# Optimization experiments

Hardware: AMD Instinct MI355X
Metric: run time of the kernel (lower is better)

The kernel has to match this reference:

```python
import jax, jax.numpy as jnp
import numpy as np

B, L, D, H, V = 4, 128, 128, 8, 32000
N_ITER = 4
DAMP_H = DAMP_Z = DAMP_X = 0.0
STEP_H = STEP_Z = STEP_X = 1.0
REG_H = REG_Z = REG_X = 1.0
BLOCK_MSG = False
NEG = 1e9


def _norm(t):
    # norm='softmax'
    return jax.nn.softmax(t, axis=-1)


def setup_inputs() -> dict:
    key = jax.random.key(0)
    k1, k2, k3, k4 = jax.random.split(key, 4)
    x = jax.random.normal(k1, (B, L, D), dtype=jnp.float32)
    mask = jnp.ones((B, L), dtype=jnp.int32)
    m_mask = jax.random.randint(k2, (B, L), 0, 2).astype(jnp.int32)
    embed_matrix = jax.random.normal(k3, (V, D), dtype=jnp.float32)
    ternary = jax.random.normal(k4, (2, D, D, H), dtype=jnp.float32)  # dists='' -> 2 groups
    return {"x": x, "mask": mask, "embed_matrix": embed_matrix, "m_mask": m_mask, "ternary": ternary}


def _forward(x, mask, embed_matrix, m_mask, ternary):
    dt = x.dtype
    mask1d = mask != 0                                   # [B,L] True = real token
    valid2d = mask1d[:, :, None] & mask1d[:, None, :]    # [B,L,L]
    inv2d = ~valid2d[:, None, :, :]                      # broadcast over heads
    keep = mask1d[..., None].astype(dt)                  # [B,L,1]
    mm = m_mask.astype(dt)[..., None]                    # [B,L,1]

    # distance mask: dists='' -> [triu(1); tril(-1)] -> [2,L,L]
    dm = jnp.triu(jnp.ones((L, L), dt), 1)
    distmask = jnp.stack([dm, dm.T], axis=0)

    eye = jnp.eye(L, dtype=dt)

    unary = x
    q_x = jnp.ones((B, L, V), dt)
    # initialize_Z=True: masked positions start from expected embedding
    pre = _norm(q_x) @ embed_matrix                      # [B,L,D]
    q_z = unary * (1.0 - mm) + pre * mm
    q_z = q_z * keep

    q_h = jnp.ones((B, H, L, L), dt) - eye * NEG
    q_h = jnp.where(inv2d, -NEG, q_h)

    cache_qh, cache_qz, cache_qx = q_h, q_z, q_x
    # async_update=True: normalize Z before first H update
    q_z = _norm(q_z) * keep

    for _ in range(N_ITER):
        # ---- H update: F[z,c,i,j] = sum_{k,a,b} q_z[z,i,a] q_z[z,j,b] T[k,a,b,c] dist[k,i,j]
        t1 = jnp.einsum('zia,kabc->zkibc', q_z, ternary)            # [B,2,L,D,H]
        F = jnp.einsum('zkibc,zjb,kij->zcij', t1, q_z, distmask)    # [B,H,L,L]
        q_h = cache_qh * DAMP_H + F * (1.0 - DAMP_H) / REG_H
        q_h = cache_qh * (1.0 - STEP_H) + q_h * STEP_H
        cache_qh = q_h
        q_h = q_h - eye * NEG
        q_h = jnp.where(inv2d, -NEG, q_h)
        q_hn = _norm(q_h)                                           # [B,H,L,L]

        # ---- Z update: first-order messages from ternary factors
        m = q_hn[:, None] * distmask[None, :, None]                 # [B,2,H,L,L]
        s1 = jnp.einsum('zkcij,zjb->zkibc', m, q_z)                 # to Z_i (head slot)
        G = jnp.einsum('zkibc,kabc->zia', s1, ternary)
        if not BLOCK_MSG:
            s2 = jnp.einsum('zkcij,zia->zkjac', m, q_z)             # to Z_j (dep slot)
            G = G + jnp.einsum('zkjac,kabc->zjb', s2, ternary)

        # unary: X message replaces word unary at <MASK> positions
        unary_eff = unary * (1.0 - mm) + (_norm(q_x) @ embed_matrix) * mm
        q_z_new = cache_qz * DAMP_Z + (unary_eff + G) * (1.0 - DAMP_Z) / REG_Z
        q_z_new = cache_qz * (1.0 - STEP_Z) + q_z_new * STEP_Z
        cache_qz = q_z_new
        q_z = _norm(q_z_new) * keep

        # ---- X update: message from Z through embedding factor
        msg_x = jnp.einsum('zia,va->ziv', q_z, embed_matrix)        # [B,L,V]
        q_x_new = cache_qx * DAMP_X + msg_x * (1.0 - DAMP_X) / REG_X
        q_x_new = cache_qx * (1.0 - STEP_X) + q_x_new * STEP_X
        cache_qx = q_x_new
        q_x = q_x_new

    # output_prob=False -> unnormalized scores
    return q_x


def reference(x, mask, embed_matrix, m_mask, ternary):
    return _forward(x, mask, embed_matrix, m_mask, ternary)
```

## Files before the change

### kernel.cpp

```cpp
#include <hip/hip_runtime.h>
#include <math.h>

#define L_ 128
#define D_ 128
#define H_ 8
#define V_ 32000
#define NEGC 1e9f

typedef short short8 __attribute__((ext_vector_type(8)));
typedef float f32x4 __attribute__((ext_vector_type(4)));
typedef unsigned short ushort8v __attribute__((ext_vector_type(8)));

__device__ __forceinline__ unsigned short f2bf(float x) {
    unsigned int u = __float_as_uint(x);
    unsigned int r = (u + 0x7fff + ((u >> 16) & 1)) >> 16;
    return (unsigned short)r;
}


__global__ __launch_bounds__(256) void prep_k(const float* __restrict__ E,
                                              unsigned short* __restrict__ Ebf,
                                              unsigned short* __restrict__ Etf,
                                              const float* __restrict__ T, float* __restrict__ Tt,
                                              const int* __restrict__ m_mask,
                                              int* __restrict__ rowidx, int* __restrict__ nactb,
                                              float* __restrict__ meansum) {
    __shared__ __align__(16) unsigned char psmem[8704];
    int blk = blockIdx.x;
    int t = threadIdx.x;
    if (blk < 1000) {
        unsigned short* tile = (unsigned short*)psmem;
        int v0 = blk * 32;
#pragma unroll
        for (int i = 0; i < 4; ++i) {
            int idx = i * 256 + t;
            int v = idx >> 5;
            int d4 = (idx & 31) * 4;
            float4 val = *(const float4*)&E[(size_t)(v0 + v) * 128 + d4];
            tile[v * 136 + d4 + 0] = f2bf(val.x);
            tile[v * 136 + d4 + 1] = f2bf(val.y);
            tile[v * 136 + d4 + 2] = f2bf(val.z);
            tile[v * 136 + d4 + 3] = f2bf(val.w);
        }
        __syncthreads();
        {
            int fi = t >> 5;
            int l0 = (t & 31) * 2;
            int vtl = fi >> 2, s = fi & 3;
            size_t base = ((size_t)(blk * 2 + vtl) * 4 + s) * 512;
#pragma unroll
            for (int li = 0; li < 2; ++li) {
                int l = l0 + li;
                int nl = l & 15, hf = l >> 4;
                ushort8v o;
#pragma unroll
                for (int j = 0; j < 8; ++j) o[j] = tile[(vtl * 16 + nl) * 136 + s * 32 + hf * 8 + j];
                *(ushort8v*)&Ebf[base + l * 8] = o;
            }
        }
        {
            int ct = t >> 5;
            int l0 = (t & 31) * 2;
            size_t base = ((size_t)blk * 8 + ct) * 512;
#pragma unroll
            for (int li = 0; li < 2; ++li) {
                int l = l0 + li;
                int nl = l & 15, hf = l >> 4;
                ushort8v o;
#pragma unroll
                for (int j = 0; j < 8; ++j) o[j] = tile[(hf * 8 + j) * 136 + ct * 16 + nl];
                *(ushort8v*)&Etf[base + l * 8] = o;
            }
        }
    } else if (blk < 1256) {
        int tb = blk - 1000;
        for (int q = 0; q < 4; ++q) {
            int id = tb * 1024 + q * 256 + t;
            int k = id >> 17;
            int rem = id & 131071;
            int a = rem >> 10;
            int bc = rem & 1023;
            int b = bc >> 3, c = bc & 7;
            Tt[k * 131072 + b * 1024 + a * 8 + c] = T[id];
        }
    } else if (blk == 1256) {
        int* wc = (int*)psmem;
        bool a0 = m_mask[t] != 0;
        bool a1 = m_mask[t + 256] != 0;
        unsigned long long b0 = __ballot(a0);
        unsigned long long b1 = __ballot(a1);
        int w = t >> 6, lane = t & 63;
        if (lane == 0) { wc[w] = __popcll(b0); wc[4 + w] = __popcll(b1); }
        __syncthreads();
        int base0 = 0;
        for (int i = 0; i < w; ++i) base0 += wc[i];
        int base1 = 0;
        for (int i = 0; i < 4 + w; ++i) base1 += wc[i];
        if (a0) rowidx[base0 + __popcll(b0 & ((1ull << lane) - 1))] = t;
        if (a1) rowidx[base1 + __popcll(b1 & ((1ull << lane) - 1))] = t + 256;
        if (t == 0) {
            int tot = 0;
            for (int i = 0; i < 8; ++i) tot += wc[i];
            nactb[0] = tot;
        }
    } else {
        float* red = (float*)psmem;
        int d = t & 127, h = t >> 7;
        int v0 = (blk - 1257) * 256;
        float s = 0.f;
        for (int p = 0; p < 128; ++p)
            s += E[(size_t)(v0 + h + 2 * p) * 128 + d];
        red[t] = s;
        __syncthreads();
        if (h == 0) atomicAdd(&meansum[d], red[d] + red[128 + d]);
    }
}

__global__ __launch_bounds__(64) void init_k(const float* __restrict__ x, const int* __restrict__ mask,
                                             const int* __restrict__ m_mask, const float* __restrict__ meansum,
                                             float* __restrict__ ue, float* __restrict__ qz,
                                             unsigned short* __restrict__ qzb) {
    int row = blockIdx.x, t = threadIdx.x;
    float keepv = mask[row] ? 1.f : 0.f;
    bool mm = m_mask[row] != 0;
    float pre0 = meansum[t] * (1.f / 32000.f);
    float pre1 = meansum[t + 64] * (1.f / 32000.f);
    float u0 = mm ? pre0 : x[row * 128 + t];
    float u1 = mm ? pre1 : x[row * 128 + t + 64];
    ue[row * 128 + t] = u0;
    ue[row * 128 + t + 64] = u1;
    float sv0 = u0 * keepv, sv1 = u1 * keepv;
    float m = fmaxf(sv0, sv1);
    for (int off = 32; off; off >>= 1) m = fmaxf(m, __shfl_xor(m, off));
    float e0 = __expf(sv0 - m), e1 = __expf(sv1 - m);
    float s = e0 + e1;
    for (int off = 32; off; off >>= 1) s += __shfl_xor(s, off);
    float inv = keepv / s;
    float q0 = e0 * inv, q1 = e1 * inv;
    qz[row * 128 + t] = q0;
    qz[row * 128 + t + 64] = q1;
    qzb[row * 128 + t] = f2bf(q0);
    qzb[row * 128 + t + 64] = f2bf(q1);
}


__global__ __launch_bounds__(256) void fusedA_k(const float* __restrict__ qz, const float* __restrict__ T,
                                                const float* __restrict__ Tt, float* __restrict__ U2,
                                                unsigned short* __restrict__ Ut, unsigned short* __restrict__ Wt,
                                                const unsigned short* __restrict__ qzb,
                                                const unsigned short* __restrict__ Ebf,
                                                const unsigned short* __restrict__ Etf,
                                                const int* __restrict__ rowidx, const int* __restrict__ nactb,
                                                float* __restrict__ partial, float* __restrict__ partial_rs) {
    __shared__ __align__(16) unsigned char smem[42752];
    int blk = blockIdx.x;
    int t = threadIdx.x;
    if (blk < 512) {
        float* aL = (float*)smem;
        int by = blk >> 5;
        int uw = by >> 3, z = (by >> 1) & 3, k = by & 1;
        int bx = blk & 31;
        int m0 = (bx >> 2) * 16, n = (bx & 3) * 256 + t;
        const float* A = qz + z * 16384;
        const float* Bm = (uw ? Tt : T) + k * 131072;
        for (int idx = t; idx < 2048; idx += 256)
            aL[idx] = A[(m0 + (idx >> 7)) * 128 + (idx & 127)];
        __syncthreads();
        float acc[16];
#pragma unroll
        for (int m = 0; m < 16; ++m) acc[m] = 0.f;
        for (int kq = 0; kq < 32; ++kq) {
            float b0 = Bm[(kq * 4 + 0) * 1024 + n];
            float b1 = Bm[(kq * 4 + 1) * 1024 + n];
            float b2 = Bm[(kq * 4 + 2) * 1024 + n];
            float b3 = Bm[(kq * 4 + 3) * 1024 + n];
#pragma unroll
            for (int m = 0; m < 16; ++m) {
                const float4 aq = *(const float4*)&aL[m * 128 + kq * 4];
                acc[m] += aq.x * b0 + aq.y * b1 + aq.z * b2 + aq.w * b3;
            }
        }
        if (uw == 0) {
            float* Cm = U2 + (z * 2 + k) * 131072;
#pragma unroll
            for (int m = 0; m < 16; ++m)
                Cm[(m0 + m) * 1024 + n] = acc[m];
        }
        int bb = n >> 3, cc = n & 7;
        ushort8v p0, p1;
#pragma unroll
        for (int m = 0; m < 8; ++m) { p0[m] = f2bf(acc[m]); p1[m] = f2bf(acc[8 + m]); }
        unsigned short* To = (uw ? Wt : Ut) + ((size_t)(z * 2 + k) * 128 + bb) * 1024 + cc * 128 + m0;
        *(ushort8v*)&To[0] = p0;
        *(ushort8v*)&To[8] = p1;
    } else {
        int nact = nactb[0];
        int bid = blk - 512;
        int xcd = bid & 7, idx = bid >> 3;
        int g = xcd + 8 * (idx >> 5);
        int bx = idx & 31;
        int r0 = bx * 16;
        if (g >= 50 || r0 >= nact) return;
        unsigned short* Pl = (unsigned short*)smem;
        float* slab = (float*)(smem + 9216);
        float* rsW  = (float*)(smem + 9216 + 33280);
        int w = t >> 6, lane = t & 63;
        int nloc = lane & 15, half = lane >> 4;
        int rA = r0 + nloc;
        bool actA = rA < nact;
        int rowA = actA ? rowidx[rA] : 0;
        short8 zero8 = (short8){0, 0, 0, 0, 0, 0, 0, 0};
        short8 afr[4];
#pragma unroll
        for (int s = 0; s < 4; ++s) {
            short8 v = *(const short8*)&qzb[rowA * 128 + s * 32 + half * 8];
            afr[s] = actA ? v : zero8;
        }
        const int kc0 = g * 20 + w * 5;
        short8 ebb[2][8];
#pragma unroll
        for (int f = 0; f < 8; ++f)
            ebb[0][f] = *(const short8*)&Ebf[((size_t)(kc0 * 8 + f)) * 512 + lane * 8];
        f32x4 acc2[8];
#pragma unroll
        for (int ct = 0; ct < 8; ++ct) acc2[ct] = (f32x4){0.f, 0.f, 0.f, 0.f};
        float rsl = 0.f;
#pragma unroll
        for (int step = 0; step < 5; ++step) {
            const int p = step & 1;
            const int kc = kc0 + step;
            short8 et[8];
#pragma unroll
            for (int f = 0; f < 8; ++f)
                et[f] = *(const short8*)&Etf[((size_t)(kc * 8 + f)) * 512 + lane * 8];
            if (step < 4) {
#pragma unroll
                for (int f = 0; f < 8; ++f)
                    ebb[p ^ 1][f] = *(const short8*)&Ebf[((size_t)((kc + 1) * 8 + f)) * 512 + lane * 8];
            }
            f32x4 p0 = (f32x4){0.f, 0.f, 0.f, 0.f};
            f32x4 p1 = (f32x4){0.f, 0.f, 0.f, 0.f};
#pragma unroll
            for (int s = 0; s < 4; ++s) {
                p0 = __builtin_amdgcn_mfma_f32_16x16x32_bf16(ebb[p][s], afr[s], p0, 0, 0, 0);
                p1 = __builtin_amdgcn_mfma_f32_16x16x32_bf16(ebb[p][4 + s], afr[s], p1, 0, 0, 0);
            }
            unsigned short* pw = Pl + (w * 2 + p) * 576;
            {
                float e0 = __expf(p0[0]), e1 = __expf(p0[1]), e2 = __expf(p0[2]), e3 = __expf(p0[3]);
                rsl += (e0 + e1) + (e2 + e3);
                uint2 pk = {(unsigned)f2bf(e0) | ((unsigned)f2bf(e1) << 16),
                            (unsigned)f2bf(e2) | ((unsigned)f2bf(e3) << 16)};
                *(uint2*)&pw[nloc * 36 + half * 4] = pk;
            }
            {
                float e0 = __expf(p1[0]), e1 = __expf(p1[1]), e2 = __expf(p1[2]), e3 = __expf(p1[3]);
                rsl += (e0 + e1) + (e2 + e3);
                uint2 pk = {(unsigned)f2bf(e0) | ((unsigned)f2bf(e1) << 16),
                            (unsigned)f2bf(e2) | ((unsigned)f2bf(e3) << 16)};
                *(uint2*)&pw[nloc * 36 + 16 + half * 4] = pk;
            }
            short8 a2 = *(const short8*)&pw[nloc * 36 + half * 8];
#pragma unroll
            for (int ct = 0; ct < 8; ++ct)
                acc2[ct] = __builtin_amdgcn_mfma_f32_16x16x32_bf16(a2, et[ct], acc2[ct], 0, 0, 0);
        }
        rsl += __shfl_xor(rsl, 16);
        rsl += __shfl_xor(rsl, 32);
        if (lane < 16) rsW[w * 16 + nloc] = rsl;
#pragma unroll
        for (int ct = 0; ct < 8; ++ct)
#pragma unroll
            for (int reg = 0; reg < 4; ++reg)
                slab[w * 2080 + (half * 4 + reg) * 130 + ct * 16 + nloc] = acc2[ct][reg];
        __syncthreads();
        float* pb = partial + (size_t)g * 65536;
        for (int i = t; i < 2048; i += 256) {
            int row = i >> 7, col = i & 127;
            int rr = r0 + row;
            if (rr < nact)
                pb[rr * 128 + col] = slab[row * 130 + col] + slab[2080 + row * 130 + col]
                                   + slab[4160 + row * 130 + col] + slab[6240 + row * 130 + col];
        }
        if (t < 16) {
            int rr = r0 + t;
            if (rr < nact)
                partial_rs[g * 512 + rr] = rsW[t] + rsW[16 + t] + rsW[32 + t] + rsW[48 + t];
        }
    }
}

__global__ __launch_bounds__(256) void fusedB_k(const float* __restrict__ qz, const float* __restrict__ U2,
                                                const int* __restrict__ mask,
                                                unsigned short* __restrict__ A0b, unsigned short* __restrict__ A1b,
                                                unsigned short* __restrict__ A0Tb, unsigned short* __restrict__ A1Tb,
                                                const float* __restrict__ partial, const float* __restrict__ partial_rs,
                                                const int* __restrict__ rowidx, const int* __restrict__ nactb,
                                                float* __restrict__ exbuf, float* __restrict__ rowsum) {
    __shared__ __align__(16) unsigned char smem[23552];
    int blk = blockIdx.x;
    int t = threadIdx.x;
    if (blk >= 256) {
        int nact = nactb[0];
        int idx = (blk - 256) * 256 + t;
        int rr = idx >> 7, col = idx & 127;
        if (rr >= nact) return;
        float s = 0.f;
#pragma unroll 10
        for (int g = 0; g < 50; ++g)
            s += partial[(size_t)g * 65536 + rr * 128 + col];
        int row = rowidx[rr];
        exbuf[row * 128 + col] = s;
        if (col == 0) {
            float ts = 0.f;
#pragma unroll 10
            for (int g = 0; g < 50; ++g) ts += partial_rs[g * 512 + rr];
            rowsum[row] = ts;
        }
        return;
    }
    float* As = (float*)smem;
    float* Bs = (float*)(smem + 4608);
    int* maskL = (int*)(smem + 4608 + 18432);
    int z = blk >> 6, c = (blk >> 3) & 7, iq = blk & 7;
    int i0 = iq * 16;
    int tj = t & 15, ti = t >> 4;
    int i = i0 + ti;
    if (t < 128) maskL[t] = mask[z * 128 + t];
    float acc0[8], acc1[8];
#pragma unroll
    for (int jj = 0; jj < 8; ++jj) { acc0[jj] = 0.f; acc1[jj] = 0.f; }
    const float* U2z = U2 + (size_t)z * 262144;
    const float* qzz = qz + z * 16384;
    for (int kb = 0; kb < 4; ++kb) {
        int b0 = kb * 32;
        __syncthreads();
        for (int e = t; e < 1024; e += 256) {
            int k = e >> 9, r = e & 511, ii = r >> 5, b = r & 31;
            As[(k * 16 + ii) * 36 + b] = U2z[k * 131072 + (i0 + ii) * 1024 + (b0 + b) * 8 + c];
        }
        for (int f = t; f < 1024; f += 256) {
            int j = f >> 3, b4 = f & 7;
            int slot = b4 ^ ((j >> 3) & 7);
            *(float4*)&Bs[j * 36 + slot * 4] = *(const float4*)&qzz[j * 128 + b0 + b4 * 4];
        }
        __syncthreads();
#pragma unroll
        for (int b4 = 0; b4 < 8; ++b4) {
            float4 a0 = *(const float4*)&As[(0 * 16 + ti) * 36 + b4 * 4];
            float4 a1 = *(const float4*)&As[(1 * 16 + ti) * 36 + b4 * 4];
#pragma unroll
            for (int jj = 0; jj < 8; ++jj) {
                int j = tj * 8 + jj;
                int slot = b4 ^ ((j >> 3) & 7);
                float4 bq = *(const float4*)&Bs[j * 36 + slot * 4];
                acc0[jj] += a0.x * bq.x;
                acc0[jj] += a0.y * bq.y;
                acc0[jj] += a0.z * bq.z;
                acc0[jj] += a0.w * bq.w;
                acc1[jj] += a1.x * bq.x;
                acc1[jj] += a1.y * bq.y;
                acc1[jj] += a1.z * bq.z;
                acc1[jj] += a1.w * bq.w;
            }
        }
    }
    bool vi = maskL[i] != 0;
    float fv[8];
#pragma unroll
    for (int jj = 0; jj < 8; ++jj) {
        int j2 = tj * 8 + jj;
        float F = (j2 > i) ? acc0[jj] : acc1[jj];
        if (j2 == i) F -= NEGC;
        if (!vi || maskL[j2] == 0) F = -NEGC;
        fv[jj] = F;
    }
    float mval = fv[0];
#pragma unroll
    for (int jj = 1; jj < 8; ++jj) mval = fmaxf(mval, fv[jj]);
    for (int off = 1; off < 16; off <<= 1) mval = fmaxf(mval, __shfl_xor(mval, off));
    float ssum = 0.f;
#pragma unroll
    for (int jj = 0; jj < 8; ++jj) ssum += __expf(fv[jj] - mval);
    for (int off = 1; off < 16; off <<= 1) ssum += __shfl_xor(ssum, off);
    float inv = 1.f / ssum;
    size_t base = (size_t)(z * 8 + c) * 16384;
    ushort8v v0, v1;
    unsigned short bvv[8];
#pragma unroll
    for (int jj = 0; jj < 8; ++jj) {
        int j2 = tj * 8 + jj;
        float val = __expf(fv[jj] - mval) * inv;
        unsigned short bv = f2bf(val);
        bvv[jj] = bv;
        v0[jj] = (j2 > i) ? bv : (unsigned short)0;
        v1[jj] = (j2 < i) ? bv : (unsigned short)0;
    }
    *(ushort8v*)&A0b[base + i * 128 + tj * 8] = v0;
    *(ushort8v*)&A1b[base + i * 128 + tj * 8] = v1;
#pragma unroll
    for (int jj = 0; jj < 8; ++jj) {
        int j2 = tj * 8 + jj;
        A0Tb[base + j2 * 128 + i] = (i < j2) ? bvv[jj] : (unsigned short)0;
        A1Tb[base + j2 * 128 + i] = (i > j2) ? bvv[jj] : (unsigned short)0;
    }
}

__global__ __launch_bounds__(64) void gkern_mfma_k(const unsigned short* __restrict__ A0b,
                                                   const unsigned short* __restrict__ A1b,
                                                   const unsigned short* __restrict__ A0Tb,
                                                   const unsigned short* __restrict__ A1Tb,
                                                   const unsigned short* __restrict__ Ut,
                                                   const unsigned short* __restrict__ Wt,
                                                   float* __restrict__ g1, float* __restrict__ g2) {
    int mode = blockIdx.y;
    int bx = blockIdx.x;
    int z = bx >> 6, it = (bx >> 3) & 7, at = bx & 7;
    int lane = threadIdx.x;
    int nloc = lane & 15, half = lane >> 4;
    int i0 = it * 16, a0 = at * 16;
    const unsigned short* Am0 = (mode ? A0Tb : A0b) + (size_t)z * 131072;
    const unsigned short* Am1 = (mode ? A1Tb : A1b) + (size_t)z * 131072;
    const unsigned short* Bt = mode ? Ut : Wt;
    const unsigned short* B0 = Bt + (size_t)(z * 2 + 0) * 131072 + (size_t)(a0 + nloc) * 1024;
    const unsigned short* B1 = Bt + (size_t)(z * 2 + 1) * 131072 + (size_t)(a0 + nloc) * 1024;
    const unsigned short* Ar0 = Am0 + (size_t)(i0 + nloc) * 128;
    const unsigned short* Ar1 = Am1 + (size_t)(i0 + nloc) * 128;
    f32x4 acc = (f32x4){0.f, 0.f, 0.f, 0.f};
#pragma unroll
    for (int c = 0; c < 8; ++c) {
#pragma unroll
        for (int sb = 0; sb < 4; ++sb) {
            int s0 = sb * 32 + half * 8;
            short8 av0 = *(const short8*)&Ar0[c * 16384 + s0];
            short8 bv0 = *(const short8*)&B0[c * 128 + s0];
            acc = __builtin_amdgcn_mfma_f32_16x16x32_bf16(av0, bv0, acc, 0, 0, 0);
            short8 av1 = *(const short8*)&Ar1[c * 16384 + s0];
            short8 bv1 = *(const short8*)&B1[c * 128 + s0];
            acc = __builtin_amdgcn_mfma_f32_16x16x32_bf16(av1, bv1, acc, 0, 0, 0);
        }
    }
    float* G = mode ? g2 : g1;
#pragma unroll
    for (int reg = 0; reg < 4; ++reg)
        G[(z * 128 + i0 + half * 4 + reg) * 128 + a0 + nloc] = acc[reg];
}

__global__ __launch_bounds__(64) void zupd_k(const float* __restrict__ ue, const float* __restrict__ x,
                                             const int* __restrict__ m_mask,
                                             const float* __restrict__ exbuf, const float* __restrict__ rowsum,
                                             const float* __restrict__ g1, const float* __restrict__ g2,
                                             const int* __restrict__ mask,
                                             float* __restrict__ qz, unsigned short* __restrict__ qzb, int useEx) {
    int row = blockIdx.x, t = threadIdx.x;
    float keepv = mask[row] ? 1.f : 0.f;
    int b = row * 128;
    float u0, u1;
    if (useEx) {
        if (m_mask[row] != 0) {
            float rsv = rowsum[row];
            u0 = exbuf[b + t] / rsv;
            u1 = exbuf[b + t + 64] / rsv;
        } else {
            u0 = x[b + t];
            u1 = x[b + t + 64];
        }
    } else {
        u0 = ue[b + t];
        u1 = ue[b + t + 64];
    }
    float v0 = u0 + g1[b + t] + g2[b + t];
    float v1 = u1 + g1[b + t + 64] + g2[b + t + 64];
    float m = fmaxf(v0, v1);
    for (int off = 32; off; off >>= 1) m = fmaxf(m, __shfl_xor(m, off));
    float e0 = __expf(v0 - m), e1 = __expf(v1 - m);
    float s = e0 + e1;
    for (int off = 32; off; off >>= 1) s += __shfl_xor(s, off);
    float inv = keepv / s;
    float q0 = e0 * inv, q1 = e1 * inv;
    qz[b + t] = q0;
    qz[b + t + 64] = q1;
    qzb[b + t] = f2bf(q0);
    qzb[b + t + 64] = f2bf(q1);
}

__global__ __launch_bounds__(256) void msgx_mfma_k(const unsigned short* __restrict__ qzb,
                                                   const unsigned short* __restrict__ Ebf,
                                                   float* __restrict__ out) {
    int t = threadIdx.x;
    int w = t >> 6, lane = t & 63;
    int nloc = lane & 15, half = lane >> 4;
    int rt0 = blockIdx.x * 64;
    int cb0 = blockIdx.y * 256 + w * 64;
    short8 afr[4][4];
#pragma unroll
    for (int r = 0; r < 4; ++r)
#pragma unroll
        for (int s = 0; s < 4; ++s)
            afr[r][s] = *(const short8*)&qzb[(rt0 + r * 16 + nloc) * 128 + s * 32 + half * 8];
    f32x4 acc[4][4];
#pragma unroll
    for (int r = 0; r < 4; ++r)
#pragma unroll
        for (int ct = 0; ct < 4; ++ct)
            acc[r][ct] = (f32x4){0.f, 0.f, 0.f, 0.f};
#pragma unroll
    for (int ct = 0; ct < 4; ++ct) {
#pragma unroll
        for (int s = 0; s < 4; ++s) {
            short8 bfr = *(const short8*)&Ebf[(((size_t)(cb0 >> 4) + ct) * 4 + s) * 512 + lane * 8];
#pragma unroll
            for (int r = 0; r < 4; ++r)
                acc[r][ct] = __builtin_amdgcn_mfma_f32_16x16x32_bf16(afr[r][s], bfr, acc[r][ct], 0, 0, 0);
        }
    }
#pragma unroll
    for (int r = 0; r < 4; ++r)
#pragma unroll
        for (int ct = 0; ct < 4; ++ct) {
            int col = cb0 + ct * 16 + nloc;
#pragma unroll
            for (int reg = 0; reg < 4; ++reg) {
                int row = rt0 + r * 16 + half * 4 + reg;
                out[(size_t)row * V_ + col] = acc[r][ct][reg];
            }
        }
}

extern "C" void kernel_launch(void* const* d_in, const int* in_sizes, int n_in,
                              void* d_out, int out_size, void* d_ws, size_t ws_size,
                              hipStream_t stream) {
    const float* x     = (const float*)d_in[0];
    const int*   mask  = (const int*)d_in[1];
    const float* E     = (const float*)d_in[2];
    const int*   mmask = (const int*)d_in[3];
    const float* T     = (const float*)d_in[4];
    float* out = (float*)d_out;

    float* w = (float*)d_ws;
    float* meansum = w;
    float* ue      = w + 128;
    float* qz      = ue + 65536;
    float* exbuf   = qz + 65536;
    float* rowsum  = exbuf + 65536;
    float* g1      = rowsum + 512;
    float* g2      = g1 + 65536;
    float* Tt      = g2 + 65536;
    float* U2      = Tt + 262144;
    float* prs     = U2 + 1048576;
    unsigned short* qzb  = (unsigned short*)(prs + 25600);
    unsigned short* Ebf  = qzb + 65536;
    unsigned short* Etf  = Ebf + 4096000;
    unsigned short* A0b  = Etf + 4096000;
    unsigned short* A1b  = A0b + 524288;
    unsigned short* A0Tb = A1b + 524288;
    unsigned short* A1Tb = A0Tb + 524288;
    unsigned short* Ut   = A1Tb + 524288;
    unsigned short* Wt   = Ut + 1048576;
    int* rowidx = (int*)(Wt + 1048576);
    int* nactb  = rowidx + 512;

    float* partial = out;

    hipMemsetAsync(meansum, 0, 128 * sizeof(float), stream);
    prep_k<<<1382, 256, 0, stream>>>(E, Ebf, Etf, T, Tt, mmask, rowidx, nactb, meansum);
    init_k<<<512, 64, 0, stream>>>(x, mask, mmask, meansum, ue, qz, qzb);

    for (int it = 0; it < 4; ++it) {
        fusedA_k<<<it ? 2304 : 512, 256, 0, stream>>>(qz, T, Tt, U2, Ut, Wt,
                                                      qzb, Ebf, Etf, rowidx, nactb, partial, prs);
        fusedB_k<<<it ? 512 : 256, 256, 0, stream>>>(qz, U2, mask, A0b, A1b, A0Tb, A1Tb,
                                                     partial, prs, rowidx, nactb, exbuf, rowsum);
        gkern_mfma_k<<<dim3(256, 2), 64, 0, stream>>>(A0b, A1b, A0Tb, A1Tb, Ut, Wt, g1, g2);
        zupd_k<<<512, 64, 0, stream>>>(ue, x, mmask, exbuf, rowsum, g1, g2, mask, qz, qzb, it ? 1 : 0);
    }
    msgx_mfma_k<<<dim3(8, 125), 256, 0, stream>>>(qzb, Ebf, out);
}
```

Before: 377.3 us.

## Double per-thread columns in fusedA GEMM and replace meansum atomics with partial sums

The fusedA GEMM branch now has each thread compute two output columns (n0 and n0+256), which halves the block count from 512 to 256 and reuses each shared-memory A load across twice the work. Separately, the embedding column-mean reduction writes per-block partial sums to a buffer instead of doing atomicAdd. init_k then sums the 125 partials itself, which also removes the memset launch. The cost is more registers per thread and fewer blocks for latency hiding, and every init block now repeats the 125-way partial sum.

```diff
diff --git a/kernel.cpp b/kernel.cpp
--- a/kernel.cpp
+++ b/kernel.cpp
@@ -24,7 +24,7 @@
                                               const float* __restrict__ T, float* __restrict__ Tt,
                                               const int* __restrict__ m_mask,
                                               int* __restrict__ rowidx, int* __restrict__ nactb,
-                                              float* __restrict__ meansum) {
+                                              float* __restrict__ cs) {
     __shared__ __align__(16) unsigned char psmem[8704];
     int blk = blockIdx.x;
     int t = threadIdx.x;
@@ -105,26 +105,33 @@
         }
     } else {
         float* red = (float*)psmem;
+        int pblk = blk - 1257;
         int d = t & 127, h = t >> 7;
-        int v0 = (blk - 1257) * 256;
+        int v0 = pblk * 256;
         float s = 0.f;
         for (int p = 0; p < 128; ++p)
             s += E[(size_t)(v0 + h + 2 * p) * 128 + d];
         red[t] = s;
         __syncthreads();
-        if (h == 0) atomicAdd(&meansum[d], red[d] + red[128 + d]);
+        if (h == 0) cs[pblk * 128 + d] = red[d] + red[128 + d];
     }
 }
 
 __global__ __launch_bounds__(64) void init_k(const float* __restrict__ x, const int* __restrict__ mask,
-                                             const int* __restrict__ m_mask, const float* __restrict__ meansum,
+                                             const int* __restrict__ m_mask, const float* __restrict__ cs,
                                              float* __restrict__ ue, float* __restrict__ qz,
                                              unsigned short* __restrict__ qzb) {
     int row = blockIdx.x, t = threadIdx.x;
     float keepv = mask[row] ? 1.f : 0.f;
     bool mm = m_mask[row] != 0;
-    float pre0 = meansum[t] * (1.f / 32000.f);
-    float pre1 = meansum[t + 64] * (1.f / 32000.f);
+    float s0 = 0.f, s1 = 0.f;
+#pragma unroll 5
+    for (int p = 0; p < 125; ++p) {
+        s0 += cs[p * 128 + t];
+        s1 += cs[p * 128 + t + 64];
+    }
+    float pre0 = s0 * (1.f / 32000.f);
+    float pre1 = s1 * (1.f / 32000.f);
     float u0 = mm ? pre0 : x[row * 128 + t];
     float u1 = mm ? pre1 : x[row * 128 + t + 64];
     ue[row * 128 + t] = u0;
@@ -155,47 +162,68 @@
     __shared__ __align__(16) unsigned char smem[42752];
     int blk = blockIdx.x;
     int t = threadIdx.x;
-    if (blk < 512) {
+    if (blk < 256) {
         float* aL = (float*)smem;
-        int by = blk >> 5;
+        int by = blk >> 4;
         int uw = by >> 3, z = (by >> 1) & 3, k = by & 1;
-        int bx = blk & 31;
-        int m0 = (bx >> 2) * 16, n = (bx & 3) * 256 + t;
+        int bx = blk & 15;
+        int m0 = (bx >> 1) * 16;
+        int n0 = (bx & 1) * 512 + t;
         const float* A = qz + z * 16384;
         const float* Bm = (uw ? Tt : T) + k * 131072;
         for (int idx = t; idx < 2048; idx += 256)
             aL[idx] = A[(m0 + (idx >> 7)) * 128 + (idx & 127)];
         __syncthreads();
-        float acc[16];
-#pragma unroll
-        for (int m = 0; m < 16; ++m) acc[m] = 0.f;
+        float acc0[16], acc1[16];
+#pragma unroll
+        for (int m = 0; m < 16; ++m) { acc0[m] = 0.f; acc1[m] = 0.f; }
         for (int kq = 0; kq < 32; ++kq) {
-            float b0 = Bm[(kq * 4 + 0) * 1024 + n];
-            float b1 = Bm[(kq * 4 + 1) * 1024 + n];
-            float b2 = Bm[(kq * 4 + 2) * 1024 + n];
-            float b3 = Bm[(kq * 4 + 3) * 1024 + n];
+            float b00 = Bm[(kq * 4 + 0) * 1024 + n0];
+            float b10 = Bm[(kq * 4 + 1) * 1024 + n0];
+            float b20 = Bm[(kq * 4 + 2) * 1024 + n0];
+            float b30 = Bm[(kq * 4 + 3) * 1024 + n0];
+            float b01 = Bm[(kq * 4 + 0) * 1024 + n0 + 256];
+            float b11 = Bm[(kq * 4 + 1) * 1024 + n0 + 256];
+            float b21 = Bm[(kq * 4 + 2) * 1024 + n0 + 256];
+            float b31 = Bm[(kq * 4 + 3) * 1024 + n0 + 256];
 #pragma unroll
             for (int m = 0; m < 16; ++m) {
                 const float4 aq = *(const float4*)&aL[m * 128 + kq * 4];
-                acc[m] += aq.x * b0 + aq.y * b1 + aq.z * b2 + aq.w * b3;
+                acc0[m] += aq.x * b00 + aq.y * b10 + aq.z * b20 + aq.w * b30;
+                acc1[m] += aq.x * b01 + aq.y * b11 + aq.z * b21 + aq.w * b31;
             }
         }
         if (uw == 0) {
             float* Cm = U2 + (z * 2 + k) * 131072;
 #pragma unroll
-            for (int m = 0; m < 16; ++m)
-                Cm[(m0 + m) * 1024 + n] = acc[m];
-        }
-        int bb = n >> 3, cc = n & 7;
-        ushort8v p0, p1;
-#pragma unroll
-        for (int m = 0; m < 8; ++m) { p0[m] = f2bf(acc[m]); p1[m] = f2bf(acc[8 + m]); }
-        unsigned short* To = (uw ? Wt : Ut) + ((size_t)(z * 2 + k) * 128 + bb) * 1024 + cc * 128 + m0;
-        *(ushort8v*)&To[0] = p0;
-        *(ushort8v*)&To[8] = p1;
+            for (int m = 0; m < 16; ++m) {
+                Cm[(m0 + m) * 1024 + n0] = acc0[m];
+                Cm[(m0 + m) * 1024 + n0 + 256] = acc1[m];
+            }
+        }
+        unsigned short* Tbase = (uw ? Wt : Ut) + (size_t)(z * 2 + k) * 131072;
+        {
+            int bb = n0 >> 3, cc = n0 & 7;
+            ushort8v p0, p1;
+#pragma unroll
+            for (int m = 0; m < 8; ++m) { p0[m] = f2bf(acc0[m]); p1[m] = f2bf(acc0[8 + m]); }
+            unsigned short* To = Tbase + (size_t)bb * 1024 + cc * 128 + m0;
+            *(ushort8v*)&To[0] = p0;
+            *(ushort8v*)&To[8] = p1;
+        }
+        {
+            int n1 = n0 + 256;
+            int bb = n1 >> 3, cc = n1 & 7;
+            ushort8v p0, p1;
+#pragma unroll
+            for (int m = 0; m < 8; ++m) { p0[m] = f2bf(acc1[m]); p1[m] = f2bf(acc1[8 + m]); }
+            unsigned short* To = Tbase + (size_t)bb * 1024 + cc * 128 + m0;
+            *(ushort8v*)&To[0] = p0;
+            *(ushort8v*)&To[8] = p1;
+        }
     } else {
         int nact = nactb[0];
-        int bid = blk - 512;
+        int bid = blk - 256;
         int xcd = bid & 7, idx = bid >> 3;
         int g = xcd + 8 * (idx >> 5);
         int bx = idx & 31;
@@ -538,8 +566,8 @@
     float* out = (float*)d_out;
 
     float* w = (float*)d_ws;
-    float* meansum = w;
-    float* ue      = w + 128;
+    float* cs      = w;
+    float* ue      = w + 16000;
     float* qz      = ue + 65536;
     float* exbuf   = qz + 65536;
     float* rowsum  = exbuf + 65536;
@@ -562,12 +590,11 @@
 
     float* partial = out;
 
-    hipMemsetAsync(meansum, 0, 128 * sizeof(float), stream);
-    prep_k<<<1382, 256, 0, stream>>>(E, Ebf, Etf, T, Tt, mmask, rowidx, nactb, meansum);
-    init_k<<<512, 64, 0, stream>>>(x, mask, mmask, meansum, ue, qz, qzb);
+    prep_k<<<1382, 256, 0, stream>>>(E, Ebf, Etf, T, Tt, mmask, rowidx, nactb, cs);
+    init_k<<<512, 64, 0, stream>>>(x, mask, mmask, cs, ue, qz, qzb);
 
     for (int it = 0; it < 4; ++it) {
-        fusedA_k<<<it ? 2304 : 512, 256, 0, stream>>>(qz, T, Tt, U2, Ut, Wt,
+        fusedA_k<<<it ? 2048 : 256, 256, 0, stream>>>(qz, T, Tt, U2, Ut, Wt,
                                                       qzb, Ebf, Etf, rowidx, nactb, partial, prs);
         fusedB_k<<<it ? 512 : 256, 256, 0, stream>>>(qz, U2, mask, A0b, A1b, A0Tb, A1Tb,
                                                      partial, prs, rowidx, nactb, exbuf, rowsum);
```

Result: no change. 370.5 us (-1.8%).
